# Kernel optimization log

Hardware: AMD Instinct MI355X
Metric: run time of the kernel (lower is better)

Reference implementation:

```python
import jax, jax.numpy as jnp
import numpy as np

# Static config (matches init_kwargs)
B, T, D = 4, 2048, 1024
E = 8            # num_experts
K = 2            # top_k
S = 1            # num_shared_experts
H = 1408         # expert_hidden_dim = round_to(4*1024//(K+S), 64)
N = B * T        # 8192 tokens
CAPACITY = 2560  # ceil(1.25 * K * N / E)
AUX_COEF = 0.01


def setup_inputs() -> dict:
    key = jax.random.key(0)
    ks = jax.random.split(key, 6)
    s = 1024 ** -0.5
    return {
        "x": jax.random.normal(ks[0], (B, T, D), jnp.float32),
        "router_weight": jax.random.normal(ks[1], (E, D), jnp.float32) * 0.02,
        "w_fc": jax.random.normal(ks[2], (E, D, H), jnp.float32) * s,
        "w_proj": jax.random.normal(ks[3], (E, H, D), jnp.float32) * s,
        "ws_fc": jax.random.normal(ks[4], (S, D, H), jnp.float32) * s,
        "ws_proj": jax.random.normal(ks[5], (S, H, D), jnp.float32) * s,
    }


def reference(x, router_weight, w_fc, w_proj, ws_fc, ws_proj):
    x_flat = x.reshape(N, D)

    # Shared experts: relu(x @ ws_fc)^2 @ ws_proj, summed over S experts
    h_s = jnp.square(jax.nn.relu(jnp.einsum("nd,sdh->snh", x_flat, ws_fc)))
    shared_out = jnp.einsum("snh,shd->nd", h_s, ws_proj)

    # Router: softmax in fp32, top-k, renormalize
    router_logits = x_flat @ router_weight.T                 # [N, E]
    routing_probs = jax.nn.softmax(router_logits.astype(jnp.float32), axis=-1)
    topk_probs, topk_idx = jax.lax.top_k(routing_probs, K)   # [N, K]
    topk_probs = topk_probs / (jnp.sum(topk_probs, axis=-1, keepdims=True) + 1e-9)
    topk_probs = topk_probs.astype(x.dtype)

    # Aux load-balancing loss (f uses top-1 assignment, no grad)
    f = jax.lax.stop_gradient(
        jnp.mean(jax.nn.one_hot(topk_idx[:, 0], E, dtype=routing_probs.dtype), axis=0))
    p = jnp.mean(routing_probs, axis=0)
    aux_loss = AUX_COEF * float(E) * jnp.sum(f * p)

    # Capacity-based dispatch: stable sort assignments by expert id
    flat_idx = topk_idx.reshape(-1)                          # [N*K]
    flat_probs = topk_probs.reshape(-1)                      # [N*K]
    flat_tok = jnp.repeat(jnp.arange(N, dtype=jnp.int32), K)  # [N*K]
    order = jnp.argsort(flat_idx, stable=True)
    sorted_idx = flat_idx[order]
    sorted_tok = flat_tok[order]
    sorted_probs = flat_probs[order]

    counts = jnp.zeros((E,), jnp.int32).at[flat_idx].add(1)
    starts = jnp.concatenate([jnp.zeros((1,), jnp.int32), jnp.cumsum(counts[:-1])])
    pos_within = jnp.arange(N * K, dtype=jnp.int32) - starts[sorted_idx]
    keep = (pos_within < CAPACITY).astype(x.dtype)
    pos_clamped = jnp.minimum(pos_within, CAPACITY - 1)
    slot = sorted_idx * CAPACITY + pos_clamped               # [N*K] -> E*CAPACITY buffer

    # Scatter tokens into per-expert capacity buffers (dropped tokens zeroed by keep)
    expert_inputs = jnp.zeros((E * CAPACITY, D), x.dtype).at[slot].add(
        x_flat[sorted_tok] * keep[:, None])
    expert_inputs = expert_inputs.reshape(E, CAPACITY, D)

    # Grouped expert FFN: relu(.)^2 MLP per expert
    hidden = jnp.square(jax.nn.relu(jnp.einsum("ecd,edh->ech", expert_inputs, w_fc)))
    expert_output = jnp.einsum("ech,ehd->ecd", hidden, w_proj).reshape(E * CAPACITY, D)

    # Gather + weighted scatter-combine back to tokens
    gathered = expert_output[slot]                           # [N*K, D]
    weighted = gathered * (sorted_probs * keep)[:, None]
    routed_out = jnp.zeros((N, D), x.dtype).at[sorted_tok].add(weighted)

    y = (routed_out + shared_out).reshape(B, T, D)
    return y, aux_loss
```

## Files before the change

kernel.cpp:

```cpp
#include <hip/hip_runtime.h>


#define NTOK 8192
#define DDIM 1024
#define HDIM 1408
#define CAP  2560
#define NROWS (NTOK + 8*CAP)
#define YN   8388608

typedef __bf16 bf16x8 __attribute__((ext_vector_type(8)));
typedef float  f32x4  __attribute__((ext_vector_type(4)));

typedef __attribute__((address_space(1))) void gvoid_t;
typedef __attribute__((address_space(3))) void svoid_t;

static __device__ __forceinline__ void load_lds16(const void* g, void* l) {
  __builtin_amdgcn_global_load_lds((gvoid_t*)g, (svoid_t*)l, 16, 0, 0);
}

__global__ __launch_bounds__(256) void tconv3_kernel(
    const float* __restrict__ wfc, __bf16* __restrict__ B1,
    const float* __restrict__ wsfc,
    const float* __restrict__ wproj, __bf16* __restrict__ B2,
    const float* __restrict__ wsproj) {
  __shared__ float t[64][33];
  int z = blockIdx.z, tid = threadIdx.x;
  const float* ip;
  __bf16* op;
  int R, C;
  if (z < 9) {
    if (blockIdx.y >= 16) return;
    R = 1024; C = 1408;
    ip = (z < 8) ? wfc + (size_t)z * R * C : wsfc;
    op = (z < 8) ? B1 + (size_t)z * (size_t)C * R : B1 + (size_t)8 * (size_t)C * R;
  } else {
    if (blockIdx.x >= 32) return;
    R = 1408; C = 1024;
    int e = z - 9;
    ip = (e < 8) ? wproj + (size_t)e * R * C : wsproj;
    op = (e < 8) ? B2 + (size_t)e * (size_t)C * R : B2 + (size_t)8 * (size_t)C * R;
  }
  int c0 = blockIdx.x * 32, r0 = blockIdx.y * 64;
  int tx = tid & 31, ty = tid >> 5;
#pragma unroll
  for (int k = 0; k < 8; ++k)
    t[ty + k * 8][tx] = ip[(size_t)(r0 + ty + k * 8) * C + c0 + tx];
  __syncthreads();
  int cl = tid >> 3, rq = (tid & 7) * 8;
  bf16x8 o;
#pragma unroll
  for (int j = 0; j < 8; ++j) o[j] = (__bf16)t[rq + j][cl];
  *(bf16x8*)(op + (size_t)(c0 + cl) * R + r0 + rq) = o;
}

__global__ __launch_bounds__(256) void router_kernel(
    const float* __restrict__ x, const float* __restrict__ rw,
    __bf16* __restrict__ xbf,
    int2* __restrict__ e01, float2* __restrict__ p01,
    int* __restrict__ tok_row, float* __restrict__ scale_row,
    float* __restrict__ psum_part, int* __restrict__ fcnt_part) {
  __shared__ float rwl[8 * 1024];
  __shared__ float ps[8];
  __shared__ int fc[8];
  int tid = threadIdx.x;
  if (tid < 8) { ps[tid] = 0.f; fc[tid] = 0; }
  float4* rl4 = (float4*)rwl;
  const float4* rg4 = (const float4*)rw;
#pragma unroll
  for (int j = 0; j < 8; ++j) rl4[tid + 256 * j] = rg4[tid + 256 * j];
  __syncthreads();
  int lane = tid & 63, wid = tid >> 6;
  for (int it = 0; it < 8; ++it) {
    int t = blockIdx.x * 32 + wid * 8 + it;
    const float4* xt = (const float4*)(x + (size_t)t * DDIM);
    float a[8];
#pragma unroll
    for (int e = 0; e < 8; ++e) a[e] = 0.f;
    float4 v[4];
#pragma unroll
    for (int jj = 0; jj < 4; ++jj) {
      v[jj] = xt[lane * 4 + jj];
#pragma unroll
      for (int e = 0; e < 8; ++e) {
        float4 w = rl4[e * 256 + lane * 4 + jj];
        a[e] += v[jj].x * w.x + v[jj].y * w.y + v[jj].z * w.z + v[jj].w * w.w;
      }
    }
    {
      bf16x8 o0, o1;
#pragma unroll
      for (int jj = 0; jj < 2; ++jj) {
        o0[jj * 4 + 0] = (__bf16)v[jj].x; o0[jj * 4 + 1] = (__bf16)v[jj].y;
        o0[jj * 4 + 2] = (__bf16)v[jj].z; o0[jj * 4 + 3] = (__bf16)v[jj].w;
        o1[jj * 4 + 0] = (__bf16)v[jj + 2].x; o1[jj * 4 + 1] = (__bf16)v[jj + 2].y;
        o1[jj * 4 + 2] = (__bf16)v[jj + 2].z; o1[jj * 4 + 3] = (__bf16)v[jj + 2].w;
      }
      __bf16* xo = xbf + (size_t)t * DDIM + lane * 16;
      *(bf16x8*)xo = o0;
      *(bf16x8*)(xo + 8) = o1;
    }
#pragma unroll
    for (int off = 32; off >= 1; off >>= 1)
#pragma unroll
      for (int e = 0; e < 8; ++e) a[e] += __shfl_xor(a[e], off);
    if (lane == 0) {
      int am = 0; float m = a[0];
      for (int e = 1; e < 8; ++e) if (a[e] > m) { m = a[e]; am = e; }
      float s = 0.f, ex[8];
      for (int e = 0; e < 8; ++e) { ex[e] = expf(a[e] - m); s += ex[e]; }
      float inv = 1.f / s;
      int am2 = -1; float m2 = -3.4e38f;
      for (int e = 0; e < 8; ++e) if (e != am && a[e] > m2) { m2 = a[e]; am2 = e; }
      float p0 = ex[am] * inv, p1 = ex[am2] * inv;
      float rn = 1.f / (p0 + p1 + 1e-9f);
      e01[t] = make_int2(am, am2);
      p01[t] = make_float2(p0 * rn, p1 * rn);
      tok_row[t] = t;
      scale_row[t] = 1.f;
      atomicAdd(&fc[am], 1);
      for (int e = 0; e < 8; ++e) atomicAdd(&ps[e], ex[e] * inv);
    }
  }
  __syncthreads();
  if (tid < 8) { psum_part[blockIdx.x * 8 + tid] = ps[tid]; fcnt_part[blockIdx.x * 8 + tid] = fc[tid]; }
}

__global__ __launch_bounds__(256) void dispatch_kernel(
    const int2* __restrict__ e01, const float2* __restrict__ p01,
    int* __restrict__ tok_row, float* __restrict__ scale_row, int* __restrict__ counts,
    const float* __restrict__ psum_part, const int* __restrict__ fcnt_part,
    float* __restrict__ aux_out) {
  __shared__ int lcnt[256][8];
  __shared__ float wps[4][8];
  __shared__ int wfcs[4][8];
  __shared__ float aps[8];
  __shared__ int afc[8];
  int tid = threadIdx.x, lane = tid & 63, w = tid >> 6;
  float s[8]; int c[8];
#pragma unroll
  for (int e = 0; e < 8; ++e) { s[e] = psum_part[tid * 8 + e]; c[e] = fcnt_part[tid * 8 + e]; }
#pragma unroll
  for (int off = 32; off >= 1; off >>= 1)
#pragma unroll
    for (int e = 0; e < 8; ++e) { s[e] += __shfl_xor(s[e], off); c[e] += __shfl_xor(c[e], off); }
  if (lane == 0) {
#pragma unroll
    for (int e = 0; e < 8; ++e) { wps[w][e] = s[e]; wfcs[w][e] = c[e]; }
  }
  int my[8];
#pragma unroll
  for (int e = 0; e < 8; ++e) my[e] = 0;
  int base = tid * 64;
  for (int j = 0; j < 64; ++j) {
    int ent = base + j; int t = ent >> 1;
    int2 ee = e01[t];
    int ex = (ent & 1) ? ee.y : ee.x;
    my[ex]++;
  }
#pragma unroll
  for (int e = 0; e < 8; ++e) lcnt[tid][e] = my[e];
  __syncthreads();
  if (tid < 8) {
    aps[tid] = wps[0][tid] + wps[1][tid] + wps[2][tid] + wps[3][tid];
    afc[tid] = wfcs[0][tid] + wfcs[1][tid] + wfcs[2][tid] + wfcs[3][tid];
    int run = 0;
    for (int i = 0; i < 256; ++i) { int cc = lcnt[i][tid]; lcnt[i][tid] = run; run += cc; }
    counts[tid] = run < CAP ? run : CAP;
  }
  __syncthreads();
  int offs[8];
#pragma unroll
  for (int e = 0; e < 8; ++e) offs[e] = lcnt[tid][e];
  for (int j = 0; j < 64; ++j) {
    int ent = base + j; int t = ent >> 1; int k = ent & 1;
    int2 ee = e01[t];
    int ex = k ? ee.y : ee.x;
    float pr = k ? p01[t].y : p01[t].x;
    int pos = offs[ex]++;
    if (pos < CAP) {
      int row = NTOK + ex * CAP + pos;
      tok_row[row] = t;
      scale_row[row] = pr;
    }
  }
  if (tid == 0) {
    float t = 0.f;
    for (int e = 0; e < 8; ++e) t += ((float)afc[e] / 8192.f) * (aps[e] / 8192.f);
    *aux_out = 0.08f * t;
  }
}

template <int KD, int NDT, bool GATHER, int EPI, int RANGE, int NT>
__global__ __launch_bounds__(256, 4) void gemm_kernel(
    const __bf16* __restrict__ A, const __bf16* __restrict__ B,
    __bf16* __restrict__ Hout, float* __restrict__ Yout,
    const int* __restrict__ counts, const int* __restrict__ tok_row,
    const float* __restrict__ scale_row) {
  constexpr int NCT = NDT / 128;
  constexpr int SH = NTOK / 128;
  constexpr int ET = CAP / 128;

  __shared__ __align__(16) __bf16 As[128 * 64];
  __shared__ __align__(16) __bf16 Bs[128 * 64];
  __shared__ int   toksL[128];
  __shared__ float sclL[128];

  int tid = threadIdx.x, lane = tid & 63, wid = tid >> 6;

  int rsub = lane >> 3, csub = lane & 7;
  int csw = (csub ^ rsub) * 16;
  int wr = wid >> 1, wc = wid & 1;
  int rA[4], rB[4], cS[2];
#pragma unroll
  for (int m2 = 0; m2 < 4; ++m2) rA[m2] = (wr * 64 + m2 * 16 + (lane & 15)) * 64;
#pragma unroll
  for (int n2 = 0; n2 < 4; ++n2) rB[n2] = (wc * 64 + n2 * 16 + (lane & 15)) * 64;
#pragma unroll
  for (int kk = 0; kk < 2; ++kk) cS[kk] = ((kk * 4 + (lane >> 4)) ^ (lane & 7)) * 8;

  for (int vt = blockIdx.x; vt < NT; vt += gridDim.x) {
    int lin = (vt & 7) * (NT >> 3) + (vt >> 3);
    int rem = lin % (4 * NCT);
    int rt = (lin / (4 * NCT)) * 4 + (rem & 3);
    int ct = rem >> 2;

    int g, i0, rowbase;
    if (RANGE == 2) { g = rt / ET; i0 = (rt % ET) << 7; rowbase = NTOK + g * CAP; }
    else {
      if (rt < SH) { g = 8; rowbase = 0; i0 = rt << 7; }
      else { int r = rt - SH; g = r / ET; i0 = (r % ET) << 7; rowbase = NTOK + g * CAP; }
    }
    int cnt = (g == 8) ? NTOK : counts[g];
    if (i0 >= cnt) continue;

    __syncthreads();
    if (tid < 128) {
      int i = i0 + tid; if (i > cnt - 1) i = cnt - 1;
      toksL[tid] = tok_row[rowbase + i];
      if (EPI == 2) sclL[tid] = scale_row[rowbase + i];
    }
    __syncthreads();

    const char* aP[4];
    const char* bP[4];
    const char* Bg = (const char*)B + (size_t)g * NDT * KD * 2;
#pragma unroll
    for (int t = 0; t < 4; ++t) {
      int ia = wid * 32 + t * 8 + rsub;
      size_t arow = GATHER ? (size_t)toksL[ia] : (size_t)(rowbase + i0 + ia);
      aP[t] = (const char*)A + arow * (size_t)(KD * 2) + csw;
      int ib = ct * 128 + wid * 32 + t * 8 + rsub;
      bP[t] = Bg + (size_t)ib * (KD * 2) + csw;
    }

    f32x4 acc[4][4];
#pragma unroll
    for (int m2 = 0; m2 < 4; ++m2)
#pragma unroll
      for (int n2 = 0; n2 < 4; ++n2) acc[m2][n2] = f32x4{0.f, 0.f, 0.f, 0.f};

    for (int k0 = 0; k0 < KD; k0 += 64) {
      size_t kb = (size_t)k0 * 2;
#pragma unroll
      for (int t = 0; t < 4; ++t) {
        load_lds16(aP[t] + kb, &As[(wid * 32 + t * 8) * 64]);
        load_lds16(bP[t] + kb, &Bs[(wid * 32 + t * 8) * 64]);
      }
      __syncthreads();
#pragma unroll
      for (int kk = 0; kk < 2; ++kk) {
        bf16x8 af[4], bfr[4];
#pragma unroll
        for (int m2 = 0; m2 < 4; ++m2) af[m2] = *(const bf16x8*)&As[rA[m2] + cS[kk]];
#pragma unroll
        for (int n2 = 0; n2 < 4; ++n2) bfr[n2] = *(const bf16x8*)&Bs[rB[n2] + cS[kk]];
#pragma unroll
        for (int m2 = 0; m2 < 4; ++m2)
#pragma unroll
          for (int n2 = 0; n2 < 4; ++n2)
            acc[m2][n2] = __builtin_amdgcn_mfma_f32_16x16x32_bf16(af[m2], bfr[n2], acc[m2][n2], 0, 0, 0);
      }
      __syncthreads();
    }

#pragma unroll
    for (int m2 = 0; m2 < 4; ++m2) {
      int rb = wr * 64 + m2 * 16 + ((lane >> 4) << 2);
#pragma unroll
      for (int n2 = 0; n2 < 4; ++n2) {
        int col = ct * 128 + wc * 64 + n2 * 16 + (lane & 15);
#pragma unroll
        for (int r = 0; r < 4; ++r) {
          int grow = i0 + rb + r;
          if (grow < cnt) {
            float v = acc[m2][n2][r];
            if constexpr (EPI == 1) {
              v = fmaxf(v, 0.f);
              Hout[(size_t)(rowbase + grow) * NDT + col] = (__bf16)(v * v);
            } else {
              atomicAdd(&Yout[(size_t)toksL[rb + r] * NDT + col], v * sclL[rb + r]);
            }
          }
        }
      }
    }
  }
}

__global__ __launch_bounds__(256, 4) void gemm2s_kernel(
    const __bf16* __restrict__ A, const __bf16* __restrict__ B,
    float* __restrict__ Yout) {
  constexpr int KD = HDIM;
  int nwg = gridDim.x;
  int lin = (blockIdx.x & 7) * (nwg >> 3) + (blockIdx.x >> 3);
  int rem = lin % 32;
  int rt = (lin / 32) * 4 + (rem & 3);
  int ct = rem >> 2;
  int i0 = rt << 6;

  __shared__ __align__(16) __bf16 As[64 * 64];
  __shared__ __align__(16) __bf16 Bs[128 * 64];

  int tid = threadIdx.x, lane = tid & 63, wid = tid >> 6;

  int rsub = lane >> 3, csub = lane & 7;
  int csw = (csub ^ rsub) * 16;
  const char* gA[2];
  const char* gB[4];
  const char* Bg = (const char*)B + (size_t)8 * DDIM * KD * 2;
#pragma unroll
  for (int q = 0; q < 2; ++q) {
    int row = (wid * 2 + q) * 8 + rsub;
    gA[q] = (const char*)A + (size_t)(i0 + row) * (KD * 2) + csw;
  }
#pragma unroll
  for (int q = 0; q < 4; ++q) {
    int row = (wid * 4 + q) * 8 + rsub;
    gB[q] = Bg + (size_t)(ct * 128 + row) * (KD * 2) + csw;
  }

  f32x4 acc[4][2];
#pragma unroll
  for (int m2 = 0; m2 < 4; ++m2)
#pragma unroll
    for (int n2 = 0; n2 < 2; ++n2) acc[m2][n2] = f32x4{0.f, 0.f, 0.f, 0.f};

  int rA[4], rB[2], cS[2];
#pragma unroll
  for (int m2 = 0; m2 < 4; ++m2) rA[m2] = (m2 * 16 + (lane & 15)) * 64;
#pragma unroll
  for (int n2 = 0; n2 < 2; ++n2) rB[n2] = (wid * 32 + n2 * 16 + (lane & 15)) * 64;
#pragma unroll
  for (int kk = 0; kk < 2; ++kk) cS[kk] = ((kk * 4 + (lane >> 4)) ^ (lane & 7)) * 8;

  for (int k0 = 0; k0 < KD; k0 += 64) {
    size_t kb = (size_t)k0 * 2;
#pragma unroll
    for (int q = 0; q < 2; ++q)
      load_lds16(gA[q] + kb, &As[((wid * 2 + q) * 8) * 64]);
#pragma unroll
    for (int q = 0; q < 4; ++q)
      load_lds16(gB[q] + kb, &Bs[((wid * 4 + q) * 8) * 64]);
    __syncthreads();
#pragma unroll
    for (int kk = 0; kk < 2; ++kk) {
      bf16x8 af[4], bfr[2];
#pragma unroll
      for (int m2 = 0; m2 < 4; ++m2) af[m2] = *(const bf16x8*)&As[rA[m2] + cS[kk]];
#pragma unroll
      for (int n2 = 0; n2 < 2; ++n2) bfr[n2] = *(const bf16x8*)&Bs[rB[n2] + cS[kk]];
#pragma unroll
      for (int m2 = 0; m2 < 4; ++m2)
#pragma unroll
        for (int n2 = 0; n2 < 2; ++n2)
          acc[m2][n2] = __builtin_amdgcn_mfma_f32_16x16x32_bf16(af[m2], bfr[n2], acc[m2][n2], 0, 0, 0);
    }
    __syncthreads();
  }

#pragma unroll
  for (int m2 = 0; m2 < 4; ++m2) {
    int rb = m2 * 16 + ((lane >> 4) << 2);
#pragma unroll
    for (int n2 = 0; n2 < 2; ++n2) {
      int col = ct * 128 + wid * 32 + n2 * 16 + (lane & 15);
#pragma unroll
      for (int r = 0; r < 4; ++r)
        Yout[(size_t)(i0 + rb + r) * DDIM + col] = acc[m2][n2][r];
    }
  }
}

extern "C" void kernel_launch(void* const* d_in, const int* in_sizes, int n_in,
                              void* d_out, int out_size, void* d_ws, size_t ws_size,
                              hipStream_t stream) {
  const float* x      = (const float*)d_in[0];
  const float* rw     = (const float*)d_in[1];
  const float* wfc    = (const float*)d_in[2];
  const float* wproj  = (const float*)d_in[3];
  const float* wsfc   = (const float*)d_in[4];
  const float* wsproj = (const float*)d_in[5];
  float* y = (float*)d_out;

  char* ws = (char*)d_ws;
  size_t off = 0;
  auto alloc = [&](size_t bytes) {
    void* p = ws + off;
    off += (bytes + 1023) & ~(size_t)1023;
    return p;
  };
  __bf16* xbf      = (__bf16*)alloc((size_t)NTOK * DDIM * 2);
  __bf16* B1       = (__bf16*)alloc((size_t)9 * HDIM * DDIM * 2);
  __bf16* B2       = (__bf16*)alloc((size_t)9 * DDIM * HDIM * 2);
  __bf16* H        = (__bf16*)alloc((size_t)NROWS * HDIM * 2);
  int*    tok_row  = (int*)alloc((size_t)NROWS * 4);
  float*  scale_row= (float*)alloc((size_t)NROWS * 4);
  int2*   e01      = (int2*)alloc((size_t)NTOK * 8);
  float2* p01      = (float2*)alloc((size_t)NTOK * 8);
  int*    counts   = (int*)alloc(1024);
  float*  psum_part= (float*)alloc(256 * 8 * 4);
  int*    fcnt_part= (int*)alloc(256 * 8 * 4);
  (void)ws_size; (void)out_size; (void)in_sizes; (void)n_in;

  tconv3_kernel<<<dim3(44, 22, 18), 256, 0, stream>>>(wfc, B1, wsfc, wproj, B2, wsproj);
  router_kernel<<<256, 256, 0, stream>>>(x, rw, xbf, e01, p01, tok_row, scale_row,
                                         psum_part, fcnt_part);
  dispatch_kernel<<<1, 256, 0, stream>>>(e01, p01, tok_row, scale_row, counts,
                                         psum_part, fcnt_part, y + YN);
  gemm_kernel<1024, 1408, true, 1, 0, 2464><<<1024, 256, 0, stream>>>(
      xbf, B1, H, nullptr, counts, tok_row, scale_row);
  gemm2s_kernel<<<1024, 256, 0, stream>>>(H, B2, y);
  gemm_kernel<1408, 1024, false, 2, 2, 1280><<<1024, 256, 0, stream>>>(
      H, B2, nullptr, y, counts, tok_row, scale_row);
}
```

Measured before the change: 302.6 us.

## Replace atomic scatter-add in expert down-projection with bf16 buffer and combine kernel

The expert down-projection GEMM no longer atomically adds scaled results into the fp32 output. It now writes unscaled bf16 rows into a per-expert buffer. A new combine kernel then reads each token's two slot indices, recorded by the dispatch kernel, and adds the scaled contributions to the shared-expert output. This removes scattered fp32 atomics and the per-tile token/scale loads for the non-gather GEMM. In exchange it adds an extra kernel launch, an intermediate bf16 write and read, and rounding of expert outputs to bf16 before combining.

```diff
diff --git a/kernel.cpp b/kernel.cpp
--- a/kernel.cpp
+++ b/kernel.cpp
@@ -9,6 +9,7 @@
 #define YN   8388608
 
 typedef __bf16 bf16x8 __attribute__((ext_vector_type(8)));
+typedef __bf16 bf16x4 __attribute__((ext_vector_type(4)));
 typedef float  f32x4  __attribute__((ext_vector_type(4)));
 
 typedef __attribute__((address_space(1))) void gvoid_t;
@@ -128,6 +129,7 @@
 __global__ __launch_bounds__(256) void dispatch_kernel(
     const int2* __restrict__ e01, const float2* __restrict__ p01,
     int* __restrict__ tok_row, float* __restrict__ scale_row, int* __restrict__ counts,
+    int* __restrict__ islot,
     const float* __restrict__ psum_part, const int* __restrict__ fcnt_part,
     float* __restrict__ aux_out) {
   __shared__ int lcnt[256][8];
@@ -181,6 +183,9 @@
       int row = NTOK + ex * CAP + pos;
       tok_row[row] = t;
       scale_row[row] = pr;
+      islot[ent] = row;
+    } else {
+      islot[ent] = -1;
     }
   }
   if (tid == 0) {
@@ -193,17 +198,15 @@
 template <int KD, int NDT, bool GATHER, int EPI, int RANGE, int NT>
 __global__ __launch_bounds__(256, 4) void gemm_kernel(
     const __bf16* __restrict__ A, const __bf16* __restrict__ B,
-    __bf16* __restrict__ Hout, float* __restrict__ Yout,
-    const int* __restrict__ counts, const int* __restrict__ tok_row,
-    const float* __restrict__ scale_row) {
+    __bf16* __restrict__ Hout,
+    const int* __restrict__ counts, const int* __restrict__ tok_row) {
   constexpr int NCT = NDT / 128;
   constexpr int SH = NTOK / 128;
   constexpr int ET = CAP / 128;
 
   __shared__ __align__(16) __bf16 As[128 * 64];
   __shared__ __align__(16) __bf16 Bs[128 * 64];
-  __shared__ int   toksL[128];
-  __shared__ float sclL[128];
+  __shared__ int toksL[128];
 
   int tid = threadIdx.x, lane = tid & 63, wid = tid >> 6;
 
@@ -233,13 +236,14 @@
     int cnt = (g == 8) ? NTOK : counts[g];
     if (i0 >= cnt) continue;
 
-    __syncthreads();
-    if (tid < 128) {
-      int i = i0 + tid; if (i > cnt - 1) i = cnt - 1;
-      toksL[tid] = tok_row[rowbase + i];
-      if (EPI == 2) sclL[tid] = scale_row[rowbase + i];
-    }
-    __syncthreads();
+    if (GATHER) {
+      __syncthreads();
+      if (tid < 128) {
+        int i = i0 + tid; if (i > cnt - 1) i = cnt - 1;
+        toksL[tid] = tok_row[rowbase + i];
+      }
+      __syncthreads();
+    }
 
     const char* aP[4];
     const char* bP[4];
@@ -298,7 +302,7 @@
               v = fmaxf(v, 0.f);
               Hout[(size_t)(rowbase + grow) * NDT + col] = (__bf16)(v * v);
             } else {
-              atomicAdd(&Yout[(size_t)toksL[rb + r] * NDT + col], v * sclL[rb + r]);
+              Hout[(size_t)(rowbase - NTOK + grow) * NDT + col] = (__bf16)v;
             }
           }
         }
@@ -389,6 +393,28 @@
         Yout[(size_t)(i0 + rb + r) * DDIM + col] = acc[m2][n2][r];
     }
   }
+}
+
+__global__ __launch_bounds__(256) void combine_kernel(
+    float* __restrict__ y, const __bf16* __restrict__ Eout,
+    const int* __restrict__ islot, const float* __restrict__ scale_row) {
+  int t = blockIdx.x, tid = threadIdx.x;
+  int s0 = islot[t * 2], s1 = islot[t * 2 + 1];
+  float4* yp = (float4*)(y + (size_t)t * DDIM) + tid;
+  float4 a = *yp;
+  if (s0 >= 0) {
+    float sc = scale_row[s0];
+    bf16x4 e = *((const bf16x4*)(Eout + (size_t)(s0 - NTOK) * DDIM) + tid);
+    a.x += sc * (float)e[0]; a.y += sc * (float)e[1];
+    a.z += sc * (float)e[2]; a.w += sc * (float)e[3];
+  }
+  if (s1 >= 0) {
+    float sc = scale_row[s1];
+    bf16x4 e = *((const bf16x4*)(Eout + (size_t)(s1 - NTOK) * DDIM) + tid);
+    a.x += sc * (float)e[0]; a.y += sc * (float)e[1];
+    a.z += sc * (float)e[2]; a.w += sc * (float)e[3];
+  }
+  *yp = a;
 }
 
 extern "C" void kernel_launch(void* const* d_in, const int* in_sizes, int n_in,
@@ -413,8 +439,10 @@
   __bf16* B1       = (__bf16*)alloc((size_t)9 * HDIM * DDIM * 2);
   __bf16* B2       = (__bf16*)alloc((size_t)9 * DDIM * HDIM * 2);
   __bf16* H        = (__bf16*)alloc((size_t)NROWS * HDIM * 2);
+  __bf16* Eout     = (__bf16*)alloc((size_t)8 * CAP * DDIM * 2);
   int*    tok_row  = (int*)alloc((size_t)NROWS * 4);
   float*  scale_row= (float*)alloc((size_t)NROWS * 4);
+  int*    islot    = (int*)alloc((size_t)NTOK * 2 * 4);
   int2*   e01      = (int2*)alloc((size_t)NTOK * 8);
   float2* p01      = (float2*)alloc((size_t)NTOK * 8);
   int*    counts   = (int*)alloc(1024);
@@ -425,11 +453,12 @@
   tconv3_kernel<<<dim3(44, 22, 18), 256, 0, stream>>>(wfc, B1, wsfc, wproj, B2, wsproj);
   router_kernel<<<256, 256, 0, stream>>>(x, rw, xbf, e01, p01, tok_row, scale_row,
                                          psum_part, fcnt_part);
-  dispatch_kernel<<<1, 256, 0, stream>>>(e01, p01, tok_row, scale_row, counts,
+  dispatch_kernel<<<1, 256, 0, stream>>>(e01, p01, tok_row, scale_row, counts, islot,
                                          psum_part, fcnt_part, y + YN);
   gemm_kernel<1024, 1408, true, 1, 0, 2464><<<1024, 256, 0, stream>>>(
-      xbf, B1, H, nullptr, counts, tok_row, scale_row);
+      xbf, B1, H, counts, tok_row);
   gemm2s_kernel<<<1024, 256, 0, stream>>>(H, B2, y);
-  gemm_kernel<1408, 1024, false, 2, 2, 1280><<<1024, 256, 0, stream>>>(
-      H, B2, nullptr, y, counts, tok_row, scale_row);
-}
+  gemm_kernel<1408, 1024, false, 4, 2, 1280><<<1024, 256, 0, stream>>>(
+      H, B2, Eout, counts, tok_row);
+  combine_kernel<<<NTOK, 256, 0, stream>>>(y, Eout, islot, scale_row);
+}
```

After: 298.8 us, median of 2. Within noise of the previous version (-1.3%).
